# Optimization experiments

Hardware: AMD Instinct MI355X
Metric: run time of the kernel (lower is better)

Reference implementation:

```python
import jax, jax.numpy as jnp
import numpy as np


def hadamard_matrix(n):
    # Recursive normalized Hadamard matrix of size 2^n (matches the torch code).
    H = np.array([[1.0]])
    for _ in range(n):
        H = np.block([[H, H], [H, -H]]) / np.sqrt(2.0)
    return jnp.asarray(H, dtype=jnp.float32)


def hadamard_conv(x, filt, bias, H):
    # x: (B, Cin, h, w); filt: (F, kh, kw); bias: (F, 1); H: (n, n)
    n = H.shape[0]
    F, kh, kw = filt.shape
    B, C = x.shape[0], x.shape[1]
    # zero-pad filters and data up to (n, n), then 2D Hadamard transform H A H
    kern = jnp.zeros((F, n, n), x.dtype).at[:, :kh, :kw].set(filt)
    kern_t = jnp.matmul(H, jnp.matmul(kern, H))            # (F, n, n)
    data = jnp.zeros((B, C, n, n), x.dtype).at[:, :, : x.shape[2], : x.shape[3]].set(x)
    data_t = jnp.matmul(H, jnp.matmul(data, H))            # (B, C, n, n)
    # Original: expand to (B, C, F, n, n), multiply by kern_t, inverse transform,
    # then sum over C. Since kern_t is independent of C and the transforms are
    # linear, sum over C first -- identical math, no huge intermediate.
    s = data_t.sum(axis=1)                                  # (B, n, n)
    prod = s[:, None, :, :] * kern_t[None, :, :, :]         # (B, F, n, n)
    out = jnp.matmul(H, jnp.matmul(prod, H))                # (B, F, n, n)
    return out + bias[:, 0][None, :, None, None]


def maxpool2(x):
    # 2x2 max pool, stride 2, on (B, C, H, W)
    return jax.lax.reduce_window(x, -jnp.inf, jax.lax.max, (1, 1, 2, 2), (1, 1, 2, 2), 'VALID')


def setup_inputs() -> dict:
    key = jax.random.key(0)
    ks = jax.random.split(key, 9)
    return {
        'x': jax.random.normal(ks[0], (2048, 3, 32, 32), dtype=jnp.float32),
        'filter1': jax.random.normal(ks[1], (32, 3, 3), dtype=jnp.float32),
        'bias1': jax.random.normal(ks[2], (32, 1), dtype=jnp.float32),
        'filter2': jax.random.normal(ks[3], (64, 3, 3), dtype=jnp.float32),
        'bias2': jax.random.normal(ks[4], (64, 1), dtype=jnp.float32),
        'fc1_w': jax.random.normal(ks[5], (512, 4096), dtype=jnp.float32) * 0.02,
        'fc1_b': jax.random.normal(ks[6], (512,), dtype=jnp.float32) * 0.02,
        'fc2_w': jax.random.normal(ks[7], (10, 512), dtype=jnp.float32) * 0.02,
        'fc2_b': jax.random.normal(ks[8], (10,), dtype=jnp.float32) * 0.02,
    }


def reference(x, filter1, bias1, filter2, bias2, fc1_w, fc1_b, fc2_w, fc2_b):
    H1 = hadamard_matrix(5)  # 32x32
    H2 = hadamard_matrix(4)  # 16x16
    out = hadamard_conv(x, filter1, bias1, H1)      # (B, 32, 32, 32)
    out = maxpool2(jax.nn.relu(out))                # (B, 32, 16, 16)
    out = hadamard_conv(out, filter2, bias2, H2)    # (B, 64, 16, 16)
    out = maxpool2(jax.nn.relu(out))                # (B, 64, 8, 8)
    out = out.reshape(-1, 4096)
    out = jax.nn.relu(out @ fc1_w.T + fc1_b)        # (B, 512)
    out = out @ fc2_w.T + fc2_b                     # (B, 10)
    return jax.nn.softmax(out, axis=1)
```

## Files before the change

kernel.cpp:

```cpp
#include <hip/hip_runtime.h>

#define DEVI __device__ __forceinline__

typedef __attribute__((ext_vector_type(8))) short short8x;
typedef __attribute__((ext_vector_type(4))) float float4x;

DEVI float shx(float v, int m) { return __shfl_xor(v, m, 64); }

DEVI unsigned bf16r(float v) {
  unsigned u = __float_as_uint(v);
  return (u + 0x7FFF + ((u >> 16) & 1)) >> 16;
}
DEVI void split2(float a, float b, unsigned& h, unsigned& l) {
  unsigned ra = bf16r(a), rb = bf16r(b);
  float fa = __uint_as_float(ra << 16), fb = __uint_as_float(rb << 16);
  unsigned la = bf16r(a - fa), lb = bf16r(b - fb);
  h = ra | (rb << 16);
  l = la | (lb << 16);
}

DEVI void gload16(const void* g, void* l) {
  __builtin_amdgcn_global_load_lds(
      (const __attribute__((address_space(1))) void*)g,
      (__attribute__((address_space(3))) void*)l, 16, 0, 0);
}

template <int N>
DEVI void fwht_local(float* v) {
#pragma unroll
  for (int s = 1; s < N; s <<= 1) {
#pragma unroll
    for (int k = 0; k < N; ++k) {
      if ((k & s) == 0) {
        float a = v[k], b = v[k | s];
        v[k] = a + b;
        v[k | s] = a - b;
      }
    }
  }
}

template <int MASK>
DEVI float lanex(float x) {
  if constexpr (MASK == 1)
    return __int_as_float(__builtin_amdgcn_update_dpp(
        0, __float_as_int(x), 0xB1, 0xF, 0xF, true));
  else if constexpr (MASK == 2)
    return __int_as_float(__builtin_amdgcn_update_dpp(
        0, __float_as_int(x), 0x4E, 0xF, 0xF, true));
  else
    return __int_as_float(__builtin_amdgcn_ds_swizzle(
        __float_as_int(x), (MASK << 10) | 0x1F));
}

template <int N, int MASK>
DEVI void xstage(float* v, bool upper) {
  const float sgn = upper ? 1.0f : -1.0f;
#pragma unroll
  for (int k = 0; k < N; ++k) {
    float u = lanex<MASK>(v[k]);
    v[k] = fmaf(sgn, v[k], u);
  }
}

template <int N>
DEVI void xbfly(float* v, int mask, int up) {
  const float sgn = up ? 1.0f : -1.0f;
#pragma unroll
  for (int k = 0; k < N; ++k) {
    float u = shx(v[k], mask);
    v[k] = fmaf(sgn, v[k], u);
  }
}

DEVI void fwht2d32(float v[16], int t) {
  fwht_local<16>(v);
  xbfly<16>(v, 1, !(t & 1));
  const int r = t >> 1;
  xbfly<16>(v, 2, !(r & 1));
  xbfly<16>(v, 4, !(r & 2));
  xbfly<16>(v, 8, !(r & 4));
  xbfly<16>(v, 16, !(r & 8));
  xbfly<16>(v, 32, !(r & 16));
}

DEVI void fwht2d16(float v[4], int l) {
  fwht_local<4>(v);
  xbfly<4>(v, 1, !(l & 1));
  xbfly<4>(v, 2, !(l & 2));
  const int r = l >> 2;
  xbfly<4>(v, 4, !(r & 1));
  xbfly<4>(v, 8, !(r & 2));
  xbfly<4>(v, 16, !(r & 4));
  xbfly<4>(v, 32, !(r & 8));
}

__global__ __launch_bounds__(64) void k_filters(
    const float* __restrict__ f1, const float* __restrict__ f2,
    float* __restrict__ kt1, float* __restrict__ kt2) {
  const int blk = blockIdx.x;
  const int t = threadIdx.x;
  if (blk < 32) {
    const int f = blk;
    const int r = t >> 1, h = t & 1;
    float v[16];
#pragma unroll
    for (int k = 0; k < 16; ++k) {
      const int c = h * 16 + k;
      v[k] = (r < 3 && c < 3) ? f1[f * 9 + r * 3 + c] : 0.0f;
    }
    fwht2d32(v, t);
#pragma unroll
    for (int k = 0; k < 16; ++k)
      kt1[f * 1024 + (h * 16 + k) * 32 + r] = v[k] * (1.0f / 32768.0f);
  } else {
    const int g = blk - 32;
    const int r = t >> 2, q = t & 3;
    float v[4];
#pragma unroll
    for (int j = 0; j < 4; ++j) {
      const int c = q * 4 + j;
      v[j] = (r < 3 && c < 3) ? f2[g * 9 + r * 3 + c] : 0.0f;
    }
    fwht2d16(v, t);
#pragma unroll
    for (int j = 0; j < 4; ++j)
      kt2[g * 256 + r * 16 + q * 4 + j] = v[j] * (1.0f / 4096.0f);
  }
}

__global__ __launch_bounds__(256) void k_conv(
    const float* __restrict__ x, const float* __restrict__ bias1,
    const float* __restrict__ bias2, const float* __restrict__ kt1,
    const float* __restrict__ kt2, unsigned short* __restrict__ Ah,
    unsigned short* __restrict__ Al) {
  __shared__ float tb[4 * 1160];
  const int b = blockIdx.x;
  const int tid = threadIdx.x;
  const int wv = tid >> 6, t = tid & 63;
  float* buf = tb + wv * 1160;
  const int wbase = 544 * (t & 1) + (t >> 1);
  const int rbase = 34 * (t >> 1) + 16 * (t & 1);

  float Ts[16];
  {
    const float* xb = x + (size_t)b * 3072 + (t >> 1) * 32 + (t & 1) * 16;
#pragma unroll
    for (int q = 0; q < 4; ++q) {
      float4 a0 = *(const float4*)(xb + 4 * q);
      float4 a1 = *(const float4*)(xb + 1024 + 4 * q);
      float4 a2 = *(const float4*)(xb + 2048 + 4 * q);
      Ts[4 * q + 0] = a0.x + a1.x + a2.x;
      Ts[4 * q + 1] = a0.y + a1.y + a2.y;
      Ts[4 * q + 2] = a0.z + a1.z + a2.z;
      Ts[4 * q + 3] = a0.w + a1.w + a2.w;
    }
  }
  fwht_local<16>(Ts);
  xstage<16, 1>(Ts, !(t & 1));
#pragma unroll
  for (int k = 0; k < 16; ++k) buf[wbase + 34 * k] = Ts[k];
  asm volatile("" ::: "memory");
#pragma unroll
  for (int j = 0; j < 8; ++j) {
    float2 v2 = *(const float2*)&buf[rbase + 2 * j];
    Ts[2 * j] = v2.x;
    Ts[2 * j + 1] = v2.y;
  }
  asm volatile("" ::: "memory");
  fwht_local<16>(Ts);
  xstage<16, 1>(Ts, !(t & 1));

  float acc[8];
#pragma unroll
  for (int j = 0; j < 8; ++j) acc[j] = 0.0f;

  for (int i = 0; i < 8; ++i) {
    const int f = wv * 8 + i;
    const float* kp = kt1 + f * 1024 + t * 16;
    float u[16];
#pragma unroll
    for (int q = 0; q < 4; ++q) {
      float4 kv = *(const float4*)(kp + 4 * q);
      u[4 * q + 0] = Ts[4 * q + 0] * kv.x;
      u[4 * q + 1] = Ts[4 * q + 1] * kv.y;
      u[4 * q + 2] = Ts[4 * q + 2] * kv.z;
      u[4 * q + 3] = Ts[4 * q + 3] * kv.w;
    }
    fwht_local<16>(u);
    xstage<16, 1>(u, !(t & 1));
#pragma unroll
    for (int k = 0; k < 16; ++k) buf[wbase + 34 * k] = u[k];
    asm volatile("" ::: "memory");
#pragma unroll
    for (int j = 0; j < 8; ++j) {
      float2 v2 = *(const float2*)&buf[rbase + 2 * j];
      u[2 * j] = v2.x;
      u[2 * j + 1] = v2.y;
    }
    asm volatile("" ::: "memory");
    fwht_local<16>(u);
    xstage<16, 1>(u, !(t & 1));
    const float bb = bias1[f];
#pragma unroll
    for (int k = 0; k < 16; ++k) u[k] = fmaxf(u[k] + bb, 0.0f);
#pragma unroll
    for (int k = 0; k < 16; ++k) u[k] = fmaxf(u[k], lanex<2>(u[k]));
#pragma unroll
    for (int j = 0; j < 8; ++j) acc[j] += fmaxf(u[2 * j], u[2 * j + 1]);
  }

  if (!(t & 2)) {
    const int pb = (t >> 2) * 20 + (t & 1) * 8;
    *(float4*)&buf[pb] = make_float4(acc[0], acc[1], acc[2], acc[3]);
    *(float4*)&buf[pb + 4] = make_float4(acc[4], acc[5], acc[6], acc[7]);
  }
  __syncthreads();

  const int f2s = t >> 4, rr = t & 15;
  float T2[16];
#pragma unroll
  for (int q = 0; q < 4; ++q) {
    float4 s = make_float4(0.f, 0.f, 0.f, 0.f);
#pragma unroll
    for (int w2 = 0; w2 < 4; ++w2) {
      const float4 v = *(const float4*)&tb[w2 * 1160 + rr * 20 + 4 * q];
      s.x += v.x; s.y += v.y; s.z += v.z; s.w += v.w;
    }
    T2[4 * q + 0] = s.x;
    T2[4 * q + 1] = s.y;
    T2[4 * q + 2] = s.z;
    T2[4 * q + 3] = s.w;
  }
  fwht_local<16>(T2);
  xstage<16, 1>(T2, !(t & 1));
  xstage<16, 2>(T2, !(t & 2));
  xstage<16, 4>(T2, !(t & 4));
  xstage<16, 8>(T2, !(t & 8));

#pragma unroll
  for (int it = 0; it < 4; ++it) {
    const int g = wv * 16 + it * 4 + f2s;
    const float* kp2 = kt2 + g * 256 + rr * 16;
    float u[16];
#pragma unroll
    for (int q = 0; q < 4; ++q) {
      float4 kv = *(const float4*)(kp2 + 4 * q);
      u[4 * q + 0] = T2[4 * q + 0] * kv.x;
      u[4 * q + 1] = T2[4 * q + 1] * kv.y;
      u[4 * q + 2] = T2[4 * q + 2] * kv.z;
      u[4 * q + 3] = T2[4 * q + 3] * kv.w;
    }
    fwht_local<16>(u);
    xstage<16, 1>(u, !(t & 1));
    xstage<16, 2>(u, !(t & 2));
    xstage<16, 4>(u, !(t & 4));
    xstage<16, 8>(u, !(t & 8));
    const float bb = bias2[g];
#pragma unroll
    for (int k = 0; k < 16; ++k) u[k] = fmaxf(u[k] + bb, 0.0f);
#pragma unroll
    for (int k = 0; k < 16; ++k) u[k] = fmaxf(u[k], lanex<1>(u[k]));
    float p[8];
#pragma unroll
    for (int j = 0; j < 8; ++j) p[j] = fmaxf(u[2 * j], u[2 * j + 1]);
    if (!(t & 1)) {
      unsigned hh[4], ll[4];
#pragma unroll
      for (int j = 0; j < 4; ++j) split2(p[2 * j], p[2 * j + 1], hh[j], ll[j]);
      const size_t off = (size_t)b * 4096 + g * 64 + (rr >> 1) * 8;
      *(uint4*)(Ah + off) = make_uint4(hh[0], hh[1], hh[2], hh[3]);
      *(uint4*)(Al + off) = make_uint4(ll[0], ll[1], ll[2], ll[3]);
    }
  }
}

__global__ __launch_bounds__(256) void k_wsplit(
    const float* __restrict__ W, unsigned short* __restrict__ Wh,
    unsigned short* __restrict__ Wl) {
  const int i = (blockIdx.x * 256 + threadIdx.x) * 4;
  float4 v = *(const float4*)(W + i);
  unsigned h0, l0, h1, l1;
  split2(v.x, v.y, h0, l0);
  split2(v.z, v.w, h1, l1);
  *(uint2*)(Wh + i) = make_uint2(h0, h1);
  *(uint2*)(Wl + i) = make_uint2(l0, l1);
}

__global__ __launch_bounds__(256) void k_fc1(
    const unsigned short* __restrict__ Ah, const unsigned short* __restrict__ Al,
    const unsigned short* __restrict__ Wh, const unsigned short* __restrict__ Wl,
    float* __restrict__ P, int M) {
  __shared__ __align__(16) unsigned char lds[49152];
  const int bid = blockIdx.x;
  const int low3 = bid & 7, rest = bid >> 3;
  const int nt = rest & 7;
  const int c = ((rest >> 3) << 3) | low3;
  const int mt = c >> 2, kidx = c & 3;
  const int m0 = mt * 128, n0 = nt * 64, k0 = kidx * 1024;

  const int tid = threadIdx.x;
  const int wv = tid >> 6, lane = tid & 63;
  const int wm = (wv >> 1) * 64, wn = (wv & 1) * 32;
  const int lm = lane & 15, lq = lane >> 4;
  const int lr = lane >> 3, lc = lane & 7;

  float4x acc[4][2];
#pragma unroll
  for (int i = 0; i < 4; ++i)
#pragma unroll
    for (int j = 0; j < 2; ++j) acc[i][j] = (float4x){0.f, 0.f, 0.f, 0.f};

  for (int kk = 0; kk < 1024; kk += 64) {
    const int kcol = k0 + kk;
#pragma unroll
    for (int it = 0; it < 4; ++it) {
      const int rbase = wv * 32 + it * 8;
      const int r = rbase + lr;
      const size_t go = (size_t)(m0 + r) * 4096 + kcol + (lc ^ (r & 7)) * 8;
      gload16(Ah + go, lds + rbase * 128);
      gload16(Al + go, lds + 16384 + rbase * 128);
    }
#pragma unroll
    for (int it = 0; it < 2; ++it) {
      const int rbase = wv * 16 + it * 8;
      const int r = rbase + lr;
      const size_t go = (size_t)(n0 + r) * 4096 + kcol + (lc ^ (r & 7)) * 8;
      gload16(Wh + go, lds + 32768 + rbase * 128);
      gload16(Wl + go, lds + 40960 + rbase * 128);
    }
    __syncthreads();

    const uint4* l4 = (const uint4*)lds;
#pragma unroll
    for (int ks = 0; ks < 2; ++ks) {
      const int ch = ks * 4 + lq;
      short8x a_h[4], a_l[4], b_h[2], b_l[2];
#pragma unroll
      for (int fm = 0; fm < 4; ++fm) {
        const int r = wm + fm * 16 + lm;
        const int s = r * 8 + (ch ^ (r & 7));
        a_h[fm] = *(const short8x*)&l4[s];
        a_l[fm] = *(const short8x*)&l4[1024 + s];
      }
#pragma unroll
      for (int fn = 0; fn < 2; ++fn) {
        const int r = wn + fn * 16 + lm;
        const int s = r * 8 + (ch ^ (r & 7));
        b_h[fn] = *(const short8x*)&l4[2048 + s];
        b_l[fn] = *(const short8x*)&l4[2560 + s];
      }
#pragma unroll
      for (int fm = 0; fm < 4; ++fm)
#pragma unroll
        for (int fn = 0; fn < 2; ++fn) {
          acc[fm][fn] = __builtin_amdgcn_mfma_f32_16x16x32_bf16(
              a_h[fm], b_h[fn], acc[fm][fn], 0, 0, 0);
          acc[fm][fn] = __builtin_amdgcn_mfma_f32_16x16x32_bf16(
              a_h[fm], b_l[fn], acc[fm][fn], 0, 0, 0);
          acc[fm][fn] = __builtin_amdgcn_mfma_f32_16x16x32_bf16(
              a_l[fm], b_h[fn], acc[fm][fn], 0, 0, 0);
        }
    }
    __syncthreads();
  }

  float* Pp = P + (size_t)kidx * ((size_t)M * 512);
#pragma unroll
  for (int fm = 0; fm < 4; ++fm)
#pragma unroll
    for (int fn = 0; fn < 2; ++fn)
#pragma unroll
      for (int i = 0; i < 4; ++i) {
        const int r = m0 + wm + fm * 16 + lq * 4 + i;
        const int cc = n0 + wn + fn * 16 + lm;
        Pp[(size_t)r * 512 + cc] = acc[fm][fn][i];
      }
}

__global__ __launch_bounds__(256) void k_fc1red4(
    const float* __restrict__ P, const float* __restrict__ bias,
    float* __restrict__ O, int total) {
  const int idx = (blockIdx.x * 256 + threadIdx.x) * 4;
  const float4 p0 = *(const float4*)(P + idx);
  const float4 p1 = *(const float4*)(P + (size_t)total + idx);
  const float4 p2 = *(const float4*)(P + (size_t)2 * total + idx);
  const float4 p3 = *(const float4*)(P + (size_t)3 * total + idx);
  const float4 bv = *(const float4*)(bias + (idx & 511));
  float4 o;
  o.x = fmaxf(p0.x + p1.x + p2.x + p3.x + bv.x, 0.0f);
  o.y = fmaxf(p0.y + p1.y + p2.y + p3.y + bv.y, 0.0f);
  o.z = fmaxf(p0.z + p1.z + p2.z + p3.z + bv.z, 0.0f);
  o.w = fmaxf(p0.w + p1.w + p2.w + p3.w + bv.w, 0.0f);
  *(float4*)(O + idx) = o;
}

__global__ __launch_bounds__(256) void k_fc2(
    const float* __restrict__ X, const float* __restrict__ W,
    const float* __restrict__ bias, float* __restrict__ out) {
  const int wv = threadIdx.x >> 6, t = threadIdx.x & 63;
  const int b = blockIdx.x * 4 + wv;
  const float* xr = X + (size_t)b * 512 + t * 8;
  const float4 x0 = *(const float4*)xr;
  const float4 x1 = *(const float4*)(xr + 4);
  float z[10];
#pragma unroll
  for (int o = 0; o < 10; ++o) {
    const float* wr = W + o * 512 + t * 8;
    const float4 w0 = *(const float4*)wr;
    const float4 w1 = *(const float4*)(wr + 4);
    float s = x0.x * w0.x;
    s = fmaf(x0.y, w0.y, s);
    s = fmaf(x0.z, w0.z, s);
    s = fmaf(x0.w, w0.w, s);
    s = fmaf(x1.x, w1.x, s);
    s = fmaf(x1.y, w1.y, s);
    s = fmaf(x1.z, w1.z, s);
    s = fmaf(x1.w, w1.w, s);
    z[o] = s;
  }
#pragma unroll
  for (int m = 1; m < 64; m <<= 1) {
#pragma unroll
    for (int o = 0; o < 10; ++o) z[o] += shx(z[o], m);
  }
#pragma unroll
  for (int o = 0; o < 10; ++o) z[o] += bias[o];
  float mx = z[0];
#pragma unroll
  for (int o = 1; o < 10; ++o) mx = fmaxf(mx, z[o]);
  float e[10];
  float ssum = 0.0f;
#pragma unroll
  for (int o = 0; o < 10; ++o) {
    e[o] = expf(z[o] - mx);
    ssum += e[o];
  }
  const float inv = 1.0f / ssum;
  if (t == 0) {
    float* dst = out + (size_t)b * 10;
#pragma unroll
    for (int o = 0; o < 10; ++o) dst[o] = e[o] * inv;
  }
}

extern "C" void kernel_launch(void* const* d_in, const int* in_sizes, int n_in,
                              void* d_out, int out_size, void* d_ws,
                              size_t ws_size, hipStream_t stream) {
  const float* x = (const float*)d_in[0];
  const float* f1 = (const float*)d_in[1];
  const float* b1 = (const float*)d_in[2];
  const float* f2 = (const float*)d_in[3];
  const float* b2 = (const float*)d_in[4];
  const float* fc1w = (const float*)d_in[5];
  const float* fc1b = (const float*)d_in[6];
  const float* fc2w = (const float*)d_in[7];
  const float* fc2b = (const float*)d_in[8];
  float* out = (float*)d_out;
  const int B = in_sizes[0] / 3072;

  char* w = (char*)d_ws;
  float* kt1 = (float*)w;
  float* kt2 = (float*)(w + 131072);
  unsigned short* Ah = (unsigned short*)(w + 196608);
  unsigned short* Al = (unsigned short*)(w + 196608 + (size_t)B * 8192);
  unsigned short* Wh = (unsigned short*)(w + 196608 + (size_t)2 * B * 8192);
  unsigned short* Wl =
      (unsigned short*)(w + 196608 + (size_t)2 * B * 8192 + 4194304);
  float* P = (float*)(w + 196608 + (size_t)2 * B * 8192 + 8388608);
  float* fc1o = (float*)(w + 196608 + (size_t)2 * B * 8192 + 8388608 +
                         (size_t)4 * B * 2048);

  hipLaunchKernelGGL(k_filters, dim3(96), dim3(64), 0, stream, f1, f2, kt1,
                     kt2);
  hipLaunchKernelGGL(k_wsplit, dim3(2048), dim3(256), 0, stream, fc1w, Wh, Wl);
  hipLaunchKernelGGL(k_conv, dim3(B), dim3(256), 0, stream, x, b1, b2, kt1,
                     kt2, Ah, Al);
  hipLaunchKernelGGL(k_fc1, dim3((B / 128) * 32), dim3(256), 0, stream, Ah, Al,
                     Wh, Wl, P, B);
  hipLaunchKernelGGL(k_fc1red4, dim3((B * 512) / 1024), dim3(256), 0, stream,
                     P, fc1b, fc1o, B * 512);
  hipLaunchKernelGGL(k_fc2, dim3(B / 4), dim3(256), 0, stream, fc1o, fc2w,
                     fc2b, out);
}
```

Baseline: 175.9 us.

## Replace Hadamard-domain convolutions with equivalent direct 3x3 dyadic stencils

The Hadamard transform, pointwise product and inverse transform reduce to a dyadic (XOR-indexed) correlation with the 3x3 filter. The conv kernel therefore computes each output as a 9-tap stencil over XOR-neighbours, using cross-lane swizzles for row neighbours and register indexing for column neighbours. This removes the FWHT butterflies, the LDS transposes, the transformed-filter precompute kernel and its global reads. The cost is a small amount of extra FMA work per output and a correctness dependence on the XOR-convolution identity and the scale factors.

```diff
diff --git a/kernel.cpp b/kernel.cpp
--- a/kernel.cpp
+++ b/kernel.cpp
@@ -23,21 +23,6 @@
   __builtin_amdgcn_global_load_lds(
       (const __attribute__((address_space(1))) void*)g,
       (__attribute__((address_space(3))) void*)l, 16, 0, 0);
-}
-
-template <int N>
-DEVI void fwht_local(float* v) {
-#pragma unroll
-  for (int s = 1; s < N; s <<= 1) {
-#pragma unroll
-    for (int k = 0; k < N; ++k) {
-      if ((k & s) == 0) {
-        float a = v[k], b = v[k | s];
-        v[k] = a + b;
-        v[k | s] = a - b;
-      }
-    }
-  }
 }
 
 template <int MASK>
@@ -53,96 +38,17 @@
         __float_as_int(x), (MASK << 10) | 0x1F));
 }
 
-template <int N, int MASK>
-DEVI void xstage(float* v, bool upper) {
-  const float sgn = upper ? 1.0f : -1.0f;
-#pragma unroll
-  for (int k = 0; k < N; ++k) {
-    float u = lanex<MASK>(v[k]);
-    v[k] = fmaf(sgn, v[k], u);
-  }
-}
-
-template <int N>
-DEVI void xbfly(float* v, int mask, int up) {
-  const float sgn = up ? 1.0f : -1.0f;
-#pragma unroll
-  for (int k = 0; k < N; ++k) {
-    float u = shx(v[k], mask);
-    v[k] = fmaf(sgn, v[k], u);
-  }
-}
-
-DEVI void fwht2d32(float v[16], int t) {
-  fwht_local<16>(v);
-  xbfly<16>(v, 1, !(t & 1));
-  const int r = t >> 1;
-  xbfly<16>(v, 2, !(r & 1));
-  xbfly<16>(v, 4, !(r & 2));
-  xbfly<16>(v, 8, !(r & 4));
-  xbfly<16>(v, 16, !(r & 8));
-  xbfly<16>(v, 32, !(r & 16));
-}
-
-DEVI void fwht2d16(float v[4], int l) {
-  fwht_local<4>(v);
-  xbfly<4>(v, 1, !(l & 1));
-  xbfly<4>(v, 2, !(l & 2));
-  const int r = l >> 2;
-  xbfly<4>(v, 4, !(r & 1));
-  xbfly<4>(v, 8, !(r & 2));
-  xbfly<4>(v, 16, !(r & 4));
-  xbfly<4>(v, 32, !(r & 8));
-}
-
-__global__ __launch_bounds__(64) void k_filters(
-    const float* __restrict__ f1, const float* __restrict__ f2,
-    float* __restrict__ kt1, float* __restrict__ kt2) {
-  const int blk = blockIdx.x;
-  const int t = threadIdx.x;
-  if (blk < 32) {
-    const int f = blk;
-    const int r = t >> 1, h = t & 1;
-    float v[16];
-#pragma unroll
-    for (int k = 0; k < 16; ++k) {
-      const int c = h * 16 + k;
-      v[k] = (r < 3 && c < 3) ? f1[f * 9 + r * 3 + c] : 0.0f;
-    }
-    fwht2d32(v, t);
-#pragma unroll
-    for (int k = 0; k < 16; ++k)
-      kt1[f * 1024 + (h * 16 + k) * 32 + r] = v[k] * (1.0f / 32768.0f);
-  } else {
-    const int g = blk - 32;
-    const int r = t >> 2, q = t & 3;
-    float v[4];
-#pragma unroll
-    for (int j = 0; j < 4; ++j) {
-      const int c = q * 4 + j;
-      v[j] = (r < 3 && c < 3) ? f2[g * 9 + r * 3 + c] : 0.0f;
-    }
-    fwht2d16(v, t);
-#pragma unroll
-    for (int j = 0; j < 4; ++j)
-      kt2[g * 256 + r * 16 + q * 4 + j] = v[j] * (1.0f / 4096.0f);
-  }
-}
-
 __global__ __launch_bounds__(256) void k_conv(
-    const float* __restrict__ x, const float* __restrict__ bias1,
-    const float* __restrict__ bias2, const float* __restrict__ kt1,
-    const float* __restrict__ kt2, unsigned short* __restrict__ Ah,
+    const float* __restrict__ x, const float* __restrict__ filt1,
+    const float* __restrict__ bias1, const float* __restrict__ filt2,
+    const float* __restrict__ bias2, unsigned short* __restrict__ Ah,
     unsigned short* __restrict__ Al) {
-  __shared__ float tb[4 * 1160];
+  __shared__ float sP[4 * 320];
   const int b = blockIdx.x;
   const int tid = threadIdx.x;
   const int wv = tid >> 6, t = tid & 63;
-  float* buf = tb + wv * 1160;
-  const int wbase = 544 * (t & 1) + (t >> 1);
-  const int rbase = 34 * (t >> 1) + 16 * (t & 1);
-
-  float Ts[16];
+
+  float s0[16];
   {
     const float* xb = x + (size_t)b * 3072 + (t >> 1) * 32 + (t & 1) * 16;
 #pragma unroll
@@ -150,60 +56,44 @@
       float4 a0 = *(const float4*)(xb + 4 * q);
       float4 a1 = *(const float4*)(xb + 1024 + 4 * q);
       float4 a2 = *(const float4*)(xb + 2048 + 4 * q);
-      Ts[4 * q + 0] = a0.x + a1.x + a2.x;
-      Ts[4 * q + 1] = a0.y + a1.y + a2.y;
-      Ts[4 * q + 2] = a0.z + a1.z + a2.z;
-      Ts[4 * q + 3] = a0.w + a1.w + a2.w;
-    }
-  }
-  fwht_local<16>(Ts);
-  xstage<16, 1>(Ts, !(t & 1));
-#pragma unroll
-  for (int k = 0; k < 16; ++k) buf[wbase + 34 * k] = Ts[k];
-  asm volatile("" ::: "memory");
-#pragma unroll
-  for (int j = 0; j < 8; ++j) {
-    float2 v2 = *(const float2*)&buf[rbase + 2 * j];
-    Ts[2 * j] = v2.x;
-    Ts[2 * j + 1] = v2.y;
-  }
-  asm volatile("" ::: "memory");
-  fwht_local<16>(Ts);
-  xstage<16, 1>(Ts, !(t & 1));
+      s0[4 * q + 0] = a0.x + a1.x + a2.x;
+      s0[4 * q + 1] = a0.y + a1.y + a2.y;
+      s0[4 * q + 2] = a0.z + a1.z + a2.z;
+      s0[4 * q + 3] = a0.w + a1.w + a2.w;
+    }
+  }
+  float s1[16], s2[16];
+#pragma unroll
+  for (int k = 0; k < 16; ++k) s1[k] = lanex<2>(s0[k]);
+#pragma unroll
+  for (int k = 0; k < 16; ++k) s2[k] = lanex<4>(s0[k]);
 
   float acc[8];
 #pragma unroll
   for (int j = 0; j < 8; ++j) acc[j] = 0.0f;
 
   for (int i = 0; i < 8; ++i) {
-    const int f = wv * 8 + i;
-    const float* kp = kt1 + f * 1024 + t * 16;
+    const int f = __builtin_amdgcn_readfirstlane(wv * 8 + i);
+    const float* fp = filt1 + f * 9;
+    float w[9];
+#pragma unroll
+    for (int k = 0; k < 9; ++k) w[k] = fp[k] * (1.0f / 32.0f);
+    const float bb = bias1[f];
     float u[16];
 #pragma unroll
-    for (int q = 0; q < 4; ++q) {
-      float4 kv = *(const float4*)(kp + 4 * q);
-      u[4 * q + 0] = Ts[4 * q + 0] * kv.x;
-      u[4 * q + 1] = Ts[4 * q + 1] * kv.y;
-      u[4 * q + 2] = Ts[4 * q + 2] * kv.z;
-      u[4 * q + 3] = Ts[4 * q + 3] * kv.w;
-    }
-    fwht_local<16>(u);
-    xstage<16, 1>(u, !(t & 1));
-#pragma unroll
-    for (int k = 0; k < 16; ++k) buf[wbase + 34 * k] = u[k];
-    asm volatile("" ::: "memory");
-#pragma unroll
-    for (int j = 0; j < 8; ++j) {
-      float2 v2 = *(const float2*)&buf[rbase + 2 * j];
-      u[2 * j] = v2.x;
-      u[2 * j + 1] = v2.y;
-    }
-    asm volatile("" ::: "memory");
-    fwht_local<16>(u);
-    xstage<16, 1>(u, !(t & 1));
-    const float bb = bias1[f];
-#pragma unroll
-    for (int k = 0; k < 16; ++k) u[k] = fmaxf(u[k] + bb, 0.0f);
+    for (int jj = 0; jj < 16; ++jj) {
+      const int j1 = jj ^ 1, j2 = jj ^ 2;
+      float v = fmaf(w[0], s0[jj], bb);
+      v = fmaf(w[1], s0[j1], v);
+      v = fmaf(w[2], s0[j2], v);
+      v = fmaf(w[3], s1[jj], v);
+      v = fmaf(w[4], s1[j1], v);
+      v = fmaf(w[5], s1[j2], v);
+      v = fmaf(w[6], s2[jj], v);
+      v = fmaf(w[7], s2[j1], v);
+      v = fmaf(w[8], s2[j2], v);
+      u[jj] = fmaxf(v, 0.0f);
+    }
 #pragma unroll
     for (int k = 0; k < 16; ++k) u[k] = fmaxf(u[k], lanex<2>(u[k]));
 #pragma unroll
@@ -211,54 +101,56 @@
   }
 
   if (!(t & 2)) {
-    const int pb = (t >> 2) * 20 + (t & 1) * 8;
-    *(float4*)&buf[pb] = make_float4(acc[0], acc[1], acc[2], acc[3]);
-    *(float4*)&buf[pb + 4] = make_float4(acc[4], acc[5], acc[6], acc[7]);
+    const int pb = wv * 320 + (t >> 2) * 20 + (t & 1) * 8;
+    *(float4*)&sP[pb] = make_float4(acc[0], acc[1], acc[2], acc[3]);
+    *(float4*)&sP[pb + 4] = make_float4(acc[4], acc[5], acc[6], acc[7]);
   }
   __syncthreads();
 
   const int f2s = t >> 4, rr = t & 15;
-  float T2[16];
+  float r0[16];
 #pragma unroll
   for (int q = 0; q < 4; ++q) {
     float4 s = make_float4(0.f, 0.f, 0.f, 0.f);
 #pragma unroll
     for (int w2 = 0; w2 < 4; ++w2) {
-      const float4 v = *(const float4*)&tb[w2 * 1160 + rr * 20 + 4 * q];
+      const float4 v = *(const float4*)&sP[w2 * 320 + rr * 20 + 4 * q];
       s.x += v.x; s.y += v.y; s.z += v.z; s.w += v.w;
     }
-    T2[4 * q + 0] = s.x;
-    T2[4 * q + 1] = s.y;
-    T2[4 * q + 2] = s.z;
-    T2[4 * q + 3] = s.w;
-  }
-  fwht_local<16>(T2);
-  xstage<16, 1>(T2, !(t & 1));
-  xstage<16, 2>(T2, !(t & 2));
-  xstage<16, 4>(T2, !(t & 4));
-  xstage<16, 8>(T2, !(t & 8));
+    r0[4 * q + 0] = s.x;
+    r0[4 * q + 1] = s.y;
+    r0[4 * q + 2] = s.z;
+    r0[4 * q + 3] = s.w;
+  }
+  float r1[16], r2[16];
+#pragma unroll
+  for (int k = 0; k < 16; ++k) r1[k] = lanex<1>(r0[k]);
+#pragma unroll
+  for (int k = 0; k < 16; ++k) r2[k] = lanex<2>(r0[k]);
 
 #pragma unroll
   for (int it = 0; it < 4; ++it) {
     const int g = wv * 16 + it * 4 + f2s;
-    const float* kp2 = kt2 + g * 256 + rr * 16;
+    const float* gp = filt2 + g * 9;
+    float w[9];
+#pragma unroll
+    for (int k = 0; k < 9; ++k) w[k] = gp[k] * (1.0f / 16.0f);
+    const float bb = bias2[g];
     float u[16];
 #pragma unroll
-    for (int q = 0; q < 4; ++q) {
-      float4 kv = *(const float4*)(kp2 + 4 * q);
-      u[4 * q + 0] = T2[4 * q + 0] * kv.x;
-      u[4 * q + 1] = T2[4 * q + 1] * kv.y;
-      u[4 * q + 2] = T2[4 * q + 2] * kv.z;
-      u[4 * q + 3] = T2[4 * q + 3] * kv.w;
-    }
-    fwht_local<16>(u);
-    xstage<16, 1>(u, !(t & 1));
-    xstage<16, 2>(u, !(t & 2));
-    xstage<16, 4>(u, !(t & 4));
-    xstage<16, 8>(u, !(t & 8));
-    const float bb = bias2[g];
-#pragma unroll
-    for (int k = 0; k < 16; ++k) u[k] = fmaxf(u[k] + bb, 0.0f);
+    for (int jj = 0; jj < 16; ++jj) {
+      const int j1 = jj ^ 1, j2 = jj ^ 2;
+      float v = fmaf(w[0], r0[jj], bb);
+      v = fmaf(w[1], r0[j1], v);
+      v = fmaf(w[2], r0[j2], v);
+      v = fmaf(w[3], r1[jj], v);
+      v = fmaf(w[4], r1[j1], v);
+      v = fmaf(w[5], r1[j2], v);
+      v = fmaf(w[6], r2[jj], v);
+      v = fmaf(w[7], r2[j1], v);
+      v = fmaf(w[8], r2[j2], v);
+      u[jj] = fmaxf(v, 0.0f);
+    }
 #pragma unroll
     for (int k = 0; k < 16; ++k) u[k] = fmaxf(u[k], lanex<1>(u[k]));
     float p[8];
@@ -460,22 +352,17 @@
   const int B = in_sizes[0] / 3072;
 
   char* w = (char*)d_ws;
-  float* kt1 = (float*)w;
-  float* kt2 = (float*)(w + 131072);
-  unsigned short* Ah = (unsigned short*)(w + 196608);
-  unsigned short* Al = (unsigned short*)(w + 196608 + (size_t)B * 8192);
-  unsigned short* Wh = (unsigned short*)(w + 196608 + (size_t)2 * B * 8192);
-  unsigned short* Wl =
-      (unsigned short*)(w + 196608 + (size_t)2 * B * 8192 + 4194304);
-  float* P = (float*)(w + 196608 + (size_t)2 * B * 8192 + 8388608);
-  float* fc1o = (float*)(w + 196608 + (size_t)2 * B * 8192 + 8388608 +
-                         (size_t)4 * B * 2048);
-
-  hipLaunchKernelGGL(k_filters, dim3(96), dim3(64), 0, stream, f1, f2, kt1,
-                     kt2);
+  unsigned short* Ah = (unsigned short*)w;
+  unsigned short* Al = (unsigned short*)(w + (size_t)B * 8192);
+  unsigned short* Wh = (unsigned short*)(w + (size_t)2 * B * 8192);
+  unsigned short* Wl = (unsigned short*)(w + (size_t)2 * B * 8192 + 4194304);
+  float* P = (float*)(w + (size_t)2 * B * 8192 + 8388608);
+  float* fc1o =
+      (float*)(w + (size_t)2 * B * 8192 + 8388608 + (size_t)4 * B * 2048);
+
   hipLaunchKernelGGL(k_wsplit, dim3(2048), dim3(256), 0, stream, fc1w, Wh, Wl);
-  hipLaunchKernelGGL(k_conv, dim3(B), dim3(256), 0, stream, x, b1, b2, kt1,
-                     kt2, Ah, Al);
+  hipLaunchKernelGGL(k_conv, dim3(B), dim3(256), 0, stream, x, f1, b1, f2, b2,
+                     Ah, Al);
   hipLaunchKernelGGL(k_fc1, dim3((B / 128) * 32), dim3(256), 0, stream, Ah, Al,
                      Wh, Wl, P, B);
   hipLaunchKernelGGL(k_fc1red4, dim3((B * 512) / 1024), dim3(256), 0, stream,
```

New measurement: 155.3 us. -11.7%, faster.
